# Kernel optimization log

Measured on AMD Instinct MI355X. Metric: run time of the kernel, lower is better.

The kernel has to match this reference:

```python
import jax, jax.numpy as jnp
import numpy as np

EPS = 1e-5

def _ln(x, g, b):
    mu = jnp.mean(x, axis=-1, keepdims=True)
    var = jnp.var(x, axis=-1, keepdims=True)
    return (x - mu) * jax.lax.rsqrt(var + EPS) * g + b

def setup_inputs() -> dict:
    key = jax.random.key(0)
    ks = jax.random.split(key, 8)
    B, L, D, H = 2, 2048, 1024, 16
    F = 4096
    s = 0.02
    return {
        "x": jax.random.normal(ks[0], (B, L, D), dtype=jnp.float32),
        "attn_mask": jnp.tril(jnp.ones((L, L), dtype=jnp.float32)),
        # weights stored [in, out] (equivalent to torch Linear weight.T)
        "w_qkuv": jax.random.normal(ks[1], (D, 4 * D), dtype=jnp.float32) * s,
        "w_out": jax.random.normal(ks[2], (D, D), dtype=jnp.float32) * s,
        "w1": jax.random.normal(ks[3], (D, F), dtype=jnp.float32) * s,
        "w2": jax.random.normal(ks[4], (F, D), dtype=jnp.float32) * s,
        "w3": jax.random.normal(ks[5], (D, F), dtype=jnp.float32) * s,
        "ln1_g": jnp.ones((D,), jnp.float32), "ln1_b": jnp.zeros((D,), jnp.float32),
        "ln2_g": jnp.ones((D,), jnp.float32), "ln2_b": jnp.zeros((D,), jnp.float32),
        "na_g": jnp.ones((D // H,), jnp.float32), "na_b": jnp.zeros((D // H,), jnp.float32),
    }

def reference(x, attn_mask, w_qkuv, w_out, w1, w2, w3,
              ln1_g, ln1_b, ln2_g, ln2_b, na_g, na_b):
    B, L, D = x.shape
    H = 16
    d = D // H
    # --- SiLU attention sublayer ---
    xn = _ln(x, ln1_g, ln1_b)
    qkuv = jax.nn.silu(xn @ w_qkuv)                       # [B, L, 4D]
    q, k, v, u = jnp.split(qkuv, 4, axis=-1)
    def heads(t):
        return t.reshape(B, L, H, d).transpose(0, 2, 1, 3)  # [B, H, L, d]
    q, k, v, u = heads(q), heads(k), heads(v), heads(u)
    scores = jnp.einsum('bhqd,bhkd->bhqk', q, k) / jnp.sqrt(jnp.float32(d))
    scores = jax.nn.silu(scores) * attn_mask              # broadcast [L, L] over B, H
    a = jnp.einsum('bhqk,bhkd->bhqd', scores, v)          # [B, H, L, d]
    a = _ln(a, na_g, na_b) * u
    a = a.transpose(0, 2, 1, 3).reshape(B, L, D)
    x = x + a @ w_out
    # --- SwiGLU FFN sublayer ---
    xn2 = _ln(x, ln2_g, ln2_b)
    x = x + (jax.nn.silu(xn2 @ w1) * (xn2 @ w3)) @ w2
    return x
```

## Files before the change

### kernel.cpp

```cpp
#include <hip/hip_runtime.h>
#include <hip/hip_bf16.h>

typedef __hip_bfloat16 bf16;
typedef __attribute__((ext_vector_type(8))) short short8;
typedef __attribute__((ext_vector_type(4))) short bfv4;
typedef __attribute__((ext_vector_type(4))) float f32x4;
typedef __attribute__((ext_vector_type(4))) unsigned short us4;

#define LN_EPS 1e-5f

__device__ __forceinline__ float siluf(float x) { return x / (1.f + __expf(-x)); }
__device__ __forceinline__ unsigned short f2bf_bits(float f) {
    bf16 h = __float2bfloat16(f);
    return *reinterpret_cast<unsigned short*>(&h);
}
__device__ __forceinline__ bf16 f2bf(float f) { return __float2bfloat16(f); }
__device__ __forceinline__ float bf2f(bf16 h) { return __bfloat162float(h); }

__device__ __forceinline__ void load_lds16(const void* g, void* l) {
    __builtin_amdgcn_global_load_lds((const __attribute__((address_space(1))) void*)g,
                                     (__attribute__((address_space(3))) void*)l, 16, 0, 0);
}

__device__ __forceinline__ f32x4 mfma16(bfv4 a, bfv4 b, f32x4 c) {
    return __builtin_amdgcn_mfma_f32_16x16x16bf16_1k(a, b, c, 0, 0, 0);
}

__device__ __forceinline__ void drain_and_sync() {
    asm volatile("s_waitcnt vmcnt(0)" ::: "memory");
    __builtin_amdgcn_sched_barrier(0);
    __syncthreads();
}

template <int N>
__device__ __forceinline__ void wait_vmcnt() {
    asm volatile("s_waitcnt vmcnt(%0)" :: "n"(N) : "memory");
}
__device__ __forceinline__ void hard_barrier() {
    __builtin_amdgcn_sched_barrier(0);
    __builtin_amdgcn_s_barrier();
    __builtin_amdgcn_sched_barrier(0);
}
__device__ __forceinline__ void lgkm_barrier() {
    asm volatile("s_waitcnt lgkmcnt(0)" ::: "memory");
    __builtin_amdgcn_sched_barrier(0);
    __builtin_amdgcn_s_barrier();
    __builtin_amdgcn_sched_barrier(0);
}

__device__ __forceinline__ int xcd_swz(int bid, int nwg) {
    return (bid & 7) * (nwg >> 3) + (bid >> 3);
}

__global__ __launch_bounds__(256) void transpose_cast(
    const float* __restrict__ src, bf16* __restrict__ dst, int K, int N)
{
    __shared__ float t[32][33];
    const int nb = blockIdx.x << 5, kb = blockIdx.y << 5;
    const int tx = threadIdx.x, ty = threadIdx.y;
#pragma unroll
    for (int i = ty; i < 32; i += 8) t[i][tx] = src[(size_t)(kb + i) * N + nb + tx];
    __syncthreads();
#pragma unroll
    for (int i = ty; i < 32; i += 8) dst[(size_t)(nb + i) * K + kb + tx] = f2bf(t[tx][i]);
}

__global__ __launch_bounds__(256) void ln_cast(
    const float* __restrict__ x, const float* __restrict__ g, const float* __restrict__ be,
    bf16* __restrict__ out)
{
    const int row = blockIdx.x, tid = threadIdx.x;
    const float4 v = ((const float4*)(x + (size_t)row * 1024))[tid];
    float s = v.x + v.y + v.z + v.w;
    float ss = v.x * v.x + v.y * v.y + v.z * v.z + v.w * v.w;
#pragma unroll
    for (int o = 32; o; o >>= 1) { s += __shfl_down(s, o); ss += __shfl_down(ss, o); }
    __shared__ float red[10];
    const int wid = tid >> 6, lane = tid & 63;
    if (lane == 0) { red[wid] = s; red[4 + wid] = ss; }
    __syncthreads();
    if (tid == 0) {
        float S = red[0] + red[1] + red[2] + red[3];
        float SS = red[4] + red[5] + red[6] + red[7];
        float mu = S * (1.f / 1024.f);
        red[8] = mu;
        red[9] = rsqrtf(SS * (1.f / 1024.f) - mu * mu + LN_EPS);
    }
    __syncthreads();
    const float mu = red[8], rstd = red[9];
    const float4 gg = ((const float4*)g)[tid];
    const float4 bb = ((const float4*)be)[tid];
    us4 o;
    o[0] = f2bf_bits((v.x - mu) * rstd * gg.x + bb.x);
    o[1] = f2bf_bits((v.y - mu) * rstd * gg.y + bb.y);
    o[2] = f2bf_bits((v.z - mu) * rstd * gg.z + bb.z);
    o[3] = f2bf_bits((v.w - mu) * rstd * gg.w + bb.w);
    ((us4*)(out + (size_t)row * 1024))[tid] = o;
}

template <int EPI>
__global__ __launch_bounds__(512, 2) void gemm8(
    const bf16* __restrict__ A, const bf16* __restrict__ BT,
    bf16* __restrict__ outp, const bf16* __restrict__ mulsrc,
    int M, int N, int K)
{
    __shared__ __align__(16) bf16 lds[2][2][256 * 64];
    const int tid = threadIdx.x;
    const int wid = tid >> 6, lane = tid & 63;
    const int lhi = lane >> 4, llo = lane & 15;
    const int ntx = N >> 8;
    const int bid = xcd_swz((int)blockIdx.x, (int)gridDim.x);
    const int bx = bid % ntx, by = bid / ntx;
    const int row0 = by << 8, col0 = bx << 8;
    const int wr = wid >> 2, wc = wid & 3;
    const int wbase = wid << 6;

    auto stage_tile = [&](const bf16* src, int r0, int k0, char* ldsbase) {
#pragma unroll
        for (int it = 0; it < 4; ++it) {
            const int p = it * 512 + wbase + lane;
            const int r = p >> 3, pc = p & 7;
            const int lc = pc ^ (r & 7);
            load_lds16(src + (size_t)(r0 + r) * K + k0 + lc * 8,
                       ldsbase + (size_t)(it * 512 + wbase) * 16);
        }
    };
    auto stageA = [&](int t) { stage_tile(A, row0, t << 6, (char*)lds[t & 1][0]); };
    auto stageB = [&](int t) { stage_tile(BT, col0, t << 6, (char*)lds[t & 1][1]); };

    f32x4 acc[8][4] = {};

    stageA(0); stageB(0); stageA(1); stageB(1);
    wait_vmcnt<8>();
    hard_barrier();

    const int KT = K >> 6;
    for (int t = 0; t < KT; ++t) {
        const int buf = t & 1;
        const char* lAc = (const char*)lds[buf][0];
        const char* lBc = (const char*)lds[buf][1];

        short8 af[4], b0[2], b1[2];
        auto ldA = [&](int mh, int kk) {
#pragma unroll
            for (int m = 0; m < 4; ++m) {
                const int ra = wr * 128 + mh * 64 + m * 16 + llo;
                af[m] = *(const short8*)(lAc + ra * 128 + (((kk * 4 + lhi) ^ (ra & 7)) << 4));
            }
        };
        auto ldB = [&](short8* bf_, int nh, int kk) {
#pragma unroll
            for (int n = 0; n < 2; ++n) {
                const int rb = wc * 64 + nh * 32 + n * 16 + llo;
                bf_[n] = *(const short8*)(lBc + rb * 128 + (((kk * 4 + lhi) ^ (rb & 7)) << 4));
            }
        };
        auto mfma_q = [&](int mh, int nh, short8* bf_) {
            __builtin_amdgcn_s_setprio(1);
#pragma unroll
            for (int m = 0; m < 4; ++m)
#pragma unroll
                for (int n = 0; n < 2; ++n)
                    acc[mh * 4 + m][nh * 2 + n] =
                        __builtin_amdgcn_mfma_f32_16x16x32_bf16(af[m], bf_[n], acc[mh * 4 + m][nh * 2 + n], 0, 0, 0);
            __builtin_amdgcn_s_setprio(0);
        };

#pragma unroll
        for (int kk = 0; kk < 2; ++kk) {
            ldA(0, kk); ldB(b0, 0, kk);
            mfma_q(0, 0, b0);
            ldB(b1, 1, kk);
            mfma_q(0, 1, b1);
            ldA(1, kk);
            mfma_q(1, 0, b0);
            mfma_q(1, 1, b1);
        }

        lgkm_barrier();
        if (t + 2 < KT) {
            stageA(t + 2); stageB(t + 2);
            wait_vmcnt<8>();
            hard_barrier();
        } else if (t + 1 < KT) {
            wait_vmcnt<0>();
            hard_barrier();
        }
    }

#pragma unroll
    for (int m = 0; m < 8; ++m) {
        const int rbase = row0 + wr * 128 + m * 16 + lhi * 4;
#pragma unroll
        for (int n = 0; n < 4; ++n) {
            const int c = col0 + wc * 64 + n * 16 + llo;
#pragma unroll
            for (int r = 0; r < 4; ++r) {
                const size_t idx = (size_t)(rbase + r) * N + c;
                const float v = acc[m][n][r];
                if constexpr (EPI == 0) outp[idx] = f2bf(siluf(v));
                else                    outp[idx] = f2bf(v * bf2f(mulsrc[idx]));
            }
        }
    }
}

__global__ __launch_bounds__(256) void gemm_btc(
    const bf16* __restrict__ A, const bf16* __restrict__ BT,
    float* __restrict__ outp, const float* __restrict__ resid,
    int M, int N, int K)
{
    __shared__ __align__(16) bf16 lA[2][128 * 64];
    __shared__ __align__(16) bf16 lB[2][64 * 64];
    const int tid = threadIdx.x;
    const int wid = tid >> 6, lane = tid & 63;
    const int lhi = lane >> 4, llo = lane & 15;
    const int ntx = N >> 6;
    const int bid = xcd_swz((int)blockIdx.x, (int)gridDim.x);
    const int bx = bid % ntx, by = bid / ntx;
    const int row0 = by << 7, col0 = bx << 6;
    const int wr = wid >> 1, wc = wid & 1;
    const int wbase = wid << 6;

    auto stage_tile = [&](const bf16* src, int r0, int k0, char* ldsbase, int nit) {
        for (int it = 0; it < nit; ++it) {
            const int p = it * 256 + wbase + lane;
            const int r = p >> 3, pc = p & 7;
            const int lc = pc ^ (r & 7);
            load_lds16(src + (size_t)(r0 + r) * K + k0 + lc * 8,
                       ldsbase + (size_t)(it * 256 + wbase) * 16);
        }
    };
    auto stageT = [&](int t) {
        stage_tile(A, row0, t << 6, (char*)lA[t & 1], 4);
        stage_tile(BT, col0, t << 6, (char*)lB[t & 1], 2);
    };

    f32x4 acc[4][2] = {};

    stageT(0); stageT(1);
    wait_vmcnt<6>();
    hard_barrier();

    const int KT = K >> 6;
    for (int t = 0; t < KT; ++t) {
        const int buf = t & 1;
        const char* lAc = (const char*)lA[buf];
        const char* lBc = (const char*)lB[buf];

        short8 af[4], bfr[2];
        auto ldA = [&](int kk) {
#pragma unroll
            for (int m = 0; m < 4; ++m) {
                const int ra = wr * 64 + m * 16 + llo;
                af[m] = *(const short8*)(lAc + ra * 128 + (((kk * 4 + lhi) ^ (ra & 7)) << 4));
            }
        };
        auto ldB = [&](int kk) {
#pragma unroll
            for (int n = 0; n < 2; ++n) {
                const int rb = wc * 32 + n * 16 + llo;
                bfr[n] = *(const short8*)(lBc + rb * 128 + (((kk * 4 + lhi) ^ (rb & 7)) << 4));
            }
        };

#pragma unroll
        for (int kk = 0; kk < 2; ++kk) {
            ldA(kk); ldB(kk);
            __builtin_amdgcn_s_setprio(1);
#pragma unroll
            for (int m = 0; m < 4; ++m)
#pragma unroll
                for (int n = 0; n < 2; ++n)
                    acc[m][n] = __builtin_amdgcn_mfma_f32_16x16x32_bf16(af[m], bfr[n], acc[m][n], 0, 0, 0);
            __builtin_amdgcn_s_setprio(0);
        }

        lgkm_barrier();
        if (t + 2 < KT) {
            stageT(t + 2);
            wait_vmcnt<6>();
            hard_barrier();
        } else if (t + 1 < KT) {
            wait_vmcnt<0>();
            hard_barrier();
        }
    }

#pragma unroll
    for (int m = 0; m < 4; ++m) {
        const int rbase = row0 + wr * 64 + m * 16 + lhi * 4;
#pragma unroll
        for (int n = 0; n < 2; ++n) {
            const int c = col0 + wc * 32 + n * 16 + llo;
#pragma unroll
            for (int r = 0; r < 4; ++r) {
                const size_t idx = (size_t)(rbase + r) * N + c;
                outp[idx] = resid[idx] + acc[m][n][r];
            }
        }
    }
}

__global__ __launch_bounds__(256) void v_trans(const bf16* __restrict__ qkuv, bf16* __restrict__ v_t)
{
    __shared__ bf16 t[64][65];
    const int bh = blockIdx.y;
    const int b = bh >> 4, h = bh & 15;
    const int l0 = blockIdx.x << 6;
    const int tx = threadIdx.x, ty = threadIdx.y;
#pragma unroll
    for (int i = ty; i < 64; i += 4)
        t[i][tx] = qkuv[(size_t)(b * 2048 + l0 + i) * 4096 + 2048 + h * 64 + tx];
    __syncthreads();
#pragma unroll
    for (int i = ty; i < 64; i += 4)
        v_t[(size_t)(bh * 64 + i) * 2048 + l0 + tx] = t[tx][i];
}

__global__ __launch_bounds__(512) void attn_kernel(
    const bf16* __restrict__ qkuv, const bf16* __restrict__ v_t,
    const float* __restrict__ nag, const float* __restrict__ nab,
    bf16* __restrict__ au)
{
    __shared__ __align__(16) bf16 lK[2][128 * 64];
    __shared__ __align__(16) bf16 lV[2][64 * 128];
    const int tid = threadIdx.x;
    const int wid = tid >> 6, lane = tid & 63;
    const int lhi = lane >> 4, llo = lane & 15;
    const int vb = xcd_swz((int)blockIdx.x, (int)gridDim.x);
    const int bh = vb >> 4;
    const int qt = 15 - (vb & 15);
    const int b = bh >> 4, h = bh & 15;
    const int q0 = qt << 7;
    const bf16* Qb = qkuv + (size_t)b * 2048 * 4096 + h * 64;
    const bf16* Kb = Qb + 1024;
    const bf16* Ub = Qb + 3072;
    const bf16* Vb = v_t + (size_t)bh * 64 * 2048;
    const int wbase = wid << 6;

    auto stage = [&](int kt_s, int buf) {
        const int koff = kt_s << 7;
        char* lKc = (char*)lK[buf];
        char* lVc = (char*)lV[buf];
#pragma unroll
        for (int it = 0; it < 2; ++it) {
            const int p = it * 512 + wbase + lane;
            const int r = p >> 3, pc = p & 7;
            const int lc = pc ^ (r & 7);
            load_lds16(Kb + (size_t)(koff + r) * 4096 + lc * 8, lKc + (it * 512 + wbase) * 16);
        }
#pragma unroll
        for (int it = 0; it < 2; ++it) {
            const int p = it * 512 + wbase + lane;
            const int d = p >> 4, pc = p & 15;
            const int lc = pc ^ (d & 15);
            load_lds16(Vb + (size_t)d * 2048 + koff + lc * 8, lVc + (it * 512 + wbase) * 16);
        }
    };

    short8 qb[2];
#pragma unroll
    for (int kk = 0; kk < 2; ++kk)
        qb[kk] = *(const short8*)(Qb + (size_t)(q0 + wid * 16 + llo) * 4096 + kk * 32 + lhi * 8);

    f32x4 acc2[4] = {};

    stage(0, 0);

    for (int kt = 0; kt <= qt; ++kt) {
        const int cur = kt & 1;
        drain_and_sync();
        if (kt < qt) stage(kt + 1, cur ^ 1);
        const char* lKc = (const char*)lK[cur];
        const char* lVc = (const char*)lV[cur];

        const bool diag = (kt == qt);
#pragma unroll
        for (int m = 0; m < 8; ++m) {
            if (diag && m > wid) break;
            const int rK = m * 16 + llo;
            const int sw = rK & 7;
            short8 ak0 = *(const short8*)(lKc + rK * 128 + ((lhi ^ sw) << 4));
            short8 ak1 = *(const short8*)(lKc + rK * 128 + (((4 + lhi) ^ sw) << 4));
            f32x4 s = {};
            s = __builtin_amdgcn_mfma_f32_16x16x32_bf16(ak0, qb[0], s, 0, 0, 0);
            s = __builtin_amdgcn_mfma_f32_16x16x32_bf16(ak1, qb[1], s, 0, 0, 0);
            const bool mask = diag && (m == wid);
            bfv4 a16;
#pragma unroll
            for (int r = 0; r < 4; ++r) {
                float xx = s[r] * 0.125f;
                xx = xx * __builtin_amdgcn_rcpf(1.f + __expf(-xx));
                if (mask && (lhi * 4 + r > llo)) xx = 0.f;
                a16[r] = (short)f2bf_bits(xx);
            }
#pragma unroll
            for (int dcol = 0; dcol < 4; ++dcol) {
                const int d = dcol * 16 + llo;
                const int lcV = m * 2 + (lhi >> 1);
                bfv4 bv = *(const bfv4*)(lVc + d * 256 + ((lcV ^ llo) << 4) + (lhi & 1) * 8);
                acc2[dcol] = mfma16(a16, bv, acc2[dcol]);
            }
        }
    }

#pragma unroll
    for (int r = 0; r < 4; ++r) {
        float vv[4];
        float s = 0.f, ss = 0.f;
#pragma unroll
        for (int dc = 0; dc < 4; ++dc) { vv[dc] = acc2[dc][r]; s += vv[dc]; ss += vv[dc] * vv[dc]; }
#pragma unroll
        for (int o = 1; o < 16; o <<= 1) { s += __shfl_xor(s, o); ss += __shfl_xor(ss, o); }
        const float mu = s * (1.f / 64.f);
        const float rstd = rsqrtf(ss * (1.f / 64.f) - mu * mu + LN_EPS);
        const int q = wid * 16 + lhi * 4 + r;
        const size_t grow = q0 + q;
#pragma unroll
        for (int dc = 0; dc < 4; ++dc) {
            const int c = dc * 16 + llo;
            const float nv = (vv[dc] - mu) * rstd * nag[c] + nab[c];
            const float uu = bf2f(Ub[grow * 4096 + c]);
            au[(size_t)(b * 2048 + grow) * 1024 + h * 64 + c] = f2bf(nv * uu);
        }
    }
}

extern "C" void kernel_launch(void* const* d_in, const int* in_sizes, int n_in,
                              void* d_out, int out_size, void* d_ws, size_t ws_size,
                              hipStream_t stream)
{
    const float* x      = (const float*)d_in[0];
    const float* w_qkuv = (const float*)d_in[2];
    const float* w_out  = (const float*)d_in[3];
    const float* w1     = (const float*)d_in[4];
    const float* w2     = (const float*)d_in[5];
    const float* w3     = (const float*)d_in[6];
    const float* ln1g   = (const float*)d_in[7];
    const float* ln1b   = (const float*)d_in[8];
    const float* ln2g   = (const float*)d_in[9];
    const float* ln2b   = (const float*)d_in[10];
    const float* nag    = (const float*)d_in[11];
    const float* nab    = (const float*)d_in[12];
    float* out = (float*)d_out;

    char* ws = (char*)d_ws;
    size_t off = 0;
    auto alloc = [&](size_t bytes) { void* p = ws + off; off += (bytes + 255) & ~(size_t)255; return p; };
    const size_t M = 4096;
    bf16* wqkuvT = (bf16*)alloc(4096ull * 1024 * 2);
    bf16* woutT  = (bf16*)alloc(1024ull * 1024 * 2);
    bf16* w1T    = (bf16*)alloc(4096ull * 1024 * 2);
    bf16* w3T    = (bf16*)alloc(4096ull * 1024 * 2);
    bf16* w2T    = (bf16*)alloc(1024ull * 4096 * 2);
    bf16* xn     = (bf16*)alloc(M * 1024 * 2);
    bf16* qkuv   = (bf16*)alloc(M * 4096 * 2);
    bf16* vt     = (bf16*)alloc(32ull * 64 * 2048 * 2);
    bf16* aub    = (bf16*)alloc(M * 1024 * 2);
    float* x2    = (float*)alloc(M * 1024 * 4);
    bf16* xn2    = (bf16*)alloc(M * 1024 * 2);
    bf16* g1     = (bf16*)alloc(M * 4096 * 2);
    bf16* h1     = (bf16*)alloc(M * 4096 * 2);
    (void)ws_size; (void)in_sizes; (void)n_in; (void)out_size;

    dim3 tb(32, 8);
    transpose_cast<<<dim3(4096 / 32, 1024 / 32), tb, 0, stream>>>(w_qkuv, wqkuvT, 1024, 4096);
    transpose_cast<<<dim3(1024 / 32, 1024 / 32), tb, 0, stream>>>(w_out, woutT, 1024, 1024);
    transpose_cast<<<dim3(4096 / 32, 1024 / 32), tb, 0, stream>>>(w1, w1T, 1024, 4096);
    transpose_cast<<<dim3(4096 / 32, 1024 / 32), tb, 0, stream>>>(w3, w3T, 1024, 4096);
    transpose_cast<<<dim3(1024 / 32, 4096 / 32), tb, 0, stream>>>(w2, w2T, 4096, 1024);

    ln_cast<<<M, 256, 0, stream>>>(x, ln1g, ln1b, xn);

    gemm8<0><<<dim3((M / 256) * (4096 / 256)), 512, 0, stream>>>(xn, wqkuvT, qkuv, nullptr, M, 4096, 1024);

    v_trans<<<dim3(2048 / 64, 32), dim3(64, 4), 0, stream>>>(qkuv, vt);

    attn_kernel<<<dim3(512), 512, 0, stream>>>(qkuv, vt, nag, nab, aub);

    gemm_btc<<<dim3((M / 128) * (1024 / 64)), 256, 0, stream>>>(aub, woutT, x2, x, M, 1024, 1024);

    ln_cast<<<M, 256, 0, stream>>>(x2, ln2g, ln2b, xn2);

    gemm8<0><<<dim3((M / 256) * (4096 / 256)), 512, 0, stream>>>(xn2, w1T, g1, nullptr, M, 4096, 1024);
    gemm8<2><<<dim3((M / 256) * (4096 / 256)), 512, 0, stream>>>(xn2, w3T, h1, g1, M, 4096, 1024);

    gemm_btc<<<dim3((M / 128) * (1024 / 64)), 256, 0, stream>>>(h1, w2T, out, x2, M, 1024, 4096);
}
```

Before: 322.3 us.

## Fuse w1 and w3 FFN GEMMs into one kernel with SwiGLU epilogue

```diff
diff --git a/kernel.cpp b/kernel.cpp
--- a/kernel.cpp
+++ b/kernel.cpp
@@ -200,6 +200,116 @@
                 const float v = acc[m][n][r];
                 if constexpr (EPI == 0) outp[idx] = f2bf(siluf(v));
                 else                    outp[idx] = f2bf(v * bf2f(mulsrc[idx]));
+            }
+        }
+    }
+}
+
+__global__ __launch_bounds__(512, 2) void gemm_w13_8(
+    const bf16* __restrict__ A, const bf16* __restrict__ B1T, const bf16* __restrict__ B3T,
+    bf16* __restrict__ outp, int M, int N, int K)
+{
+    __shared__ __align__(16) bf16 lA[2][256 * 64];
+    __shared__ __align__(16) bf16 lB1[2][128 * 64];
+    __shared__ __align__(16) bf16 lB3[2][128 * 64];
+    const int tid = threadIdx.x;
+    const int wid = tid >> 6, lane = tid & 63;
+    const int lhi = lane >> 4, llo = lane & 15;
+    const int ntx = N >> 7;
+    const int bid = xcd_swz((int)blockIdx.x, (int)gridDim.x);
+    const int bx = bid % ntx, by = bid / ntx;
+    const int row0 = by << 8, col0 = bx << 7;
+    const int wr = wid >> 2, wc = wid & 3;
+    const int wbase = wid << 6;
+
+    auto stage_rows = [&](const bf16* src, int r0, int k0, char* ldsbase, int nit) {
+        for (int it = 0; it < nit; ++it) {
+            const int p = it * 512 + wbase + lane;
+            const int r = p >> 3, pc = p & 7;
+            const int lc = pc ^ (r & 7);
+            load_lds16(src + (size_t)(r0 + r) * K + k0 + lc * 8,
+                       ldsbase + (size_t)(it * 512 + wbase) * 16);
+        }
+    };
+    auto stageT = [&](int t) {
+        const int k0 = t << 6, buf = t & 1;
+        stage_rows(A, row0, k0, (char*)lA[buf], 4);
+        stage_rows(B1T, col0, k0, (char*)lB1[buf], 2);
+        stage_rows(B3T, col0, k0, (char*)lB3[buf], 2);
+    };
+
+    f32x4 acc1[8][2] = {}, acc3[8][2] = {};
+
+    stageT(0); stageT(1);
+    wait_vmcnt<8>();
+    hard_barrier();
+
+    const int KT = K >> 6;
+    for (int t = 0; t < KT; ++t) {
+        const int buf = t & 1;
+        const char* lAc = (const char*)lA[buf];
+        const char* lB1c = (const char*)lB1[buf];
+        const char* lB3c = (const char*)lB3[buf];
+
+        short8 af[4], b1[2], b3[2];
+        auto ldA = [&](int mh, int kk) {
+#pragma unroll
+            for (int m = 0; m < 4; ++m) {
+                const int ra = wr * 128 + mh * 64 + m * 16 + llo;
+                af[m] = *(const short8*)(lAc + ra * 128 + (((kk * 4 + lhi) ^ (ra & 7)) << 4));
+            }
+        };
+        auto ldB = [&](int kk) {
+#pragma unroll
+            for (int n = 0; n < 2; ++n) {
+                const int rb = wc * 32 + n * 16 + llo;
+                const int so = (((kk * 4 + lhi) ^ (rb & 7)) << 4);
+                b1[n] = *(const short8*)(lB1c + rb * 128 + so);
+                b3[n] = *(const short8*)(lB3c + rb * 128 + so);
+            }
+        };
+        auto mfma_h = [&](int mh) {
+            __builtin_amdgcn_s_setprio(1);
+#pragma unroll
+            for (int m = 0; m < 4; ++m)
+#pragma unroll
+                for (int n = 0; n < 2; ++n) {
+                    acc1[mh * 4 + m][n] = __builtin_amdgcn_mfma_f32_16x16x32_bf16(af[m], b1[n], acc1[mh * 4 + m][n], 0, 0, 0);
+                    acc3[mh * 4 + m][n] = __builtin_amdgcn_mfma_f32_16x16x32_bf16(af[m], b3[n], acc3[mh * 4 + m][n], 0, 0, 0);
+                }
+            __builtin_amdgcn_s_setprio(0);
+        };
+
+#pragma unroll
+        for (int kk = 0; kk < 2; ++kk) {
+            ldB(kk);
+            ldA(0, kk);
+            mfma_h(0);
+            ldA(1, kk);
+            mfma_h(1);
+        }
+
+        lgkm_barrier();
+        if (t + 2 < KT) {
+            stageT(t + 2);
+            wait_vmcnt<8>();
+            hard_barrier();
+        } else if (t + 1 < KT) {
+            wait_vmcnt<0>();
+            hard_barrier();
+        }
+    }
+
+#pragma unroll
+    for (int m = 0; m < 8; ++m) {
+        const int rbase = row0 + wr * 128 + m * 16 + lhi * 4;
+#pragma unroll
+        for (int n = 0; n < 2; ++n) {
+            const int c = col0 + wc * 32 + n * 16 + llo;
+#pragma unroll
+            for (int r = 0; r < 4; ++r) {
+                const size_t idx = (size_t)(rbase + r) * N + c;
+                outp[idx] = f2bf(siluf(acc1[m][n][r]) * acc3[m][n][r]);
             }
         }
     }
@@ -460,7 +570,6 @@
     bf16* aub    = (bf16*)alloc(M * 1024 * 2);
     float* x2    = (float*)alloc(M * 1024 * 4);
     bf16* xn2    = (bf16*)alloc(M * 1024 * 2);
-    bf16* g1     = (bf16*)alloc(M * 4096 * 2);
     bf16* h1     = (bf16*)alloc(M * 4096 * 2);
     (void)ws_size; (void)in_sizes; (void)n_in; (void)out_size;
 
@@ -483,8 +592,7 @@
 
     ln_cast<<<M, 256, 0, stream>>>(x2, ln2g, ln2b, xn2);
 
-    gemm8<0><<<dim3((M / 256) * (4096 / 256)), 512, 0, stream>>>(xn2, w1T, g1, nullptr, M, 4096, 1024);
-    gemm8<2><<<dim3((M / 256) * (4096 / 256)), 512, 0, stream>>>(xn2, w3T, h1, g1, M, 4096, 1024);
+    gemm_w13_8<<<dim3((M / 256) * (4096 / 128)), 512, 0, stream>>>(xn2, w1T, w3T, h1, M, 4096, 1024);
 
     gemm_btc<<<dim3((M / 128) * (1024 / 64)), 256, 0, stream>>>(h1, w2T, out, x2, M, 1024, 4096);
 }
```

Measured after the change: 307.4 us. -4.6%, faster.
